# Performance work log

Measured on AMD Instinct MI355X. Metric: run time of the kernel, lower is better.

## Reference

```python
import jax, jax.numpy as jnp
import numpy as np

K = 3
STRIDE = 1
PAD = 1
DIL = 1


def setup_inputs() -> dict:
    key = jax.random.key(0)
    k1, k2, k3 = jax.random.split(key, 3)
    B, C, O, H, W = 8, 64, 64, 128, 128
    x = jax.random.normal(k1, (B, C, H, W), dtype=jnp.float32)
    # small offset-conv weights so predicted offsets stay in a sane range
    w_off = jax.random.normal(k2, (2 * K * K, C, K, K), dtype=jnp.float32) * 0.05
    b_off = jnp.zeros((2 * K * K,), dtype=jnp.float32)
    w_conv = jax.random.normal(k3, (O, C, K, K), dtype=jnp.float32) * (1.0 / np.sqrt(C * K * K))
    return {"x": x, "w_off": w_off, "b_off": b_off, "w_conv": w_conv}


def _offset_conv(x, w, b):
    y = jax.lax.conv_general_dilated(
        x, w, window_strides=(STRIDE, STRIDE),
        padding=[(PAD, PAD), (PAD, PAD)], rhs_dilation=(DIL, DIL),
        dimension_numbers=("NCHW", "OIHW", "NCHW"))
    return y + b[None, :, None, None]


def _deform_conv2d(x, offset, weight):
    # torchvision deform_conv2d v1, groups=1, offset_groups=1, no bias
    B, C, H, W = x.shape
    Ho, Wo = offset.shape[2], offset.shape[3]
    # offset channels laid out as (ky, kx, [dy, dx]) pairs
    off = offset.reshape(B, K, K, 2, Ho, Wo)
    dy, dx = off[:, :, :, 0], off[:, :, :, 1]           # [B,K,K,Ho,Wo]

    hs = (jnp.arange(Ho) * STRIDE - PAD).astype(offset.dtype)
    ws = (jnp.arange(Wo) * STRIDE - PAD).astype(offset.dtype)
    kk = (jnp.arange(K) * DIL).astype(offset.dtype)
    py = hs[None, None, None, :, None] + kk[None, :, None, None, None] + dy
    px = ws[None, None, None, None, :] + kk[None, None, :, None, None] + dx

    y0 = jnp.floor(py)
    x0 = jnp.floor(px)
    ly = py - y0
    lx = px - x0
    y0i = y0.astype(jnp.int32)
    x0i = x0.astype(jnp.int32)

    xf = x.reshape(B, C, H * W)

    def gather(yi, xi):
        valid = ((yi >= 0) & (yi < H) & (xi >= 0) & (xi < W)).astype(x.dtype)
        idx = jnp.clip(yi, 0, H - 1) * W + jnp.clip(xi, 0, W - 1)  # [B,K,K,Ho,Wo]
        idxf = idx.reshape(B, 1, -1)
        v = jnp.take_along_axis(xf, idxf, axis=2)                  # [B,C,K*K*Ho*Wo]
        v = v.reshape(B, C, K, K, Ho, Wo)
        return v * valid[:, None]                                  # zero-pad out of bounds

    ly_ = ly[:, None]  # broadcast over channel dim
    lx_ = lx[:, None]
    val = (gather(y0i, x0i) * (1 - ly_) * (1 - lx_)
           + gather(y0i, x0i + 1) * (1 - ly_) * lx_
           + gather(y0i + 1, x0i) * ly_ * (1 - lx_)
           + gather(y0i + 1, x0i + 1) * ly_ * lx_)   # [B,C,K,K,Ho,Wo]

    return jnp.einsum("bcklhw,ockl->bohw", val, weight)


def reference(x, w_off, b_off, w_conv):
    offset = _offset_conv(x, w_off, b_off)
    return _deform_conv2d(x, offset, w_conv)
```

## Files before the change

### kernel.cpp

```cpp
#include <hip/hip_runtime.h>

#define B_    8
#define C_    64
#define O_    64
#define H_    128
#define W_    128
#define HW_   (H_ * W_)
#define NOFF_ 18
#define KK_   9

typedef __attribute__((ext_vector_type(8))) _Float16 f16x8;
typedef __attribute__((ext_vector_type(2))) _Float16 f16x2;
typedef __attribute__((ext_vector_type(4))) unsigned int u32x4;
typedef __attribute__((ext_vector_type(4))) float f32x4;
typedef unsigned int uint32;
typedef unsigned short ushort;

__device__ __forceinline__ f16x2 u2h(uint32 u) {
    union { uint32 u; f16x2 h; } c; c.u = u; return c.h;
}
__device__ __forceinline__ f16x8 u2h8(u32x4 q) {
    union { u32x4 u; f16x8 h; } c; c.u = q; return c.h;
}

#define GLOAD16(dst, a64) \
    asm volatile("global_load_dwordx4 %0, %1, off" : "=&v"(dst) : "v"(a64) : "memory")
#define WAITV(N) do { \
    asm volatile("s_waitcnt vmcnt(" #N ")" ::: "memory"); \
    __builtin_amdgcn_sched_barrier(0); } while (0)
#define WAITLGKM0() do { \
    asm volatile("s_waitcnt lgkmcnt(0)" ::: "memory"); \
    __builtin_amdgcn_sched_barrier(0); } while (0)
#define DRAIN_ALL() do { \
    asm volatile("s_waitcnt vmcnt(0) lgkmcnt(0)" ::: "memory"); \
    __builtin_amdgcn_sched_barrier(0); } while (0)

__global__ __launch_bounds__(256) void transpose_x(
    const float* __restrict__ x, _Float16* __restrict__ xT)
{
    __shared__ float tile[64][65];
    int blk = blockIdx.x;
    int b   = blk >> 8;
    int hw0 = (blk & 255) * 64;
    int t   = threadIdx.x;
    int q   = t >> 6;
    int ln  = t & 63;
#pragma unroll
    for (int p = 0; p < 16; ++p) {
        int c = p * 4 + q;
        tile[c][ln] = x[((size_t)(b * C_ + c) << 14) + hw0 + ln];
    }
    __syncthreads();
#pragma unroll
    for (int p = 0; p < 16; ++p) {
        int hw = p * 4 + q;
        xT[(((size_t)b << 14) + hw0 + hw) * 64 + ln] = (_Float16)tile[ln][hw];
    }
}

__global__ __launch_bounds__(256) void prep3(
    const float* __restrict__ w_conv, const float* __restrict__ w_off,
    _Float16* __restrict__ wfrag, _Float16* __restrict__ wofff)
{
    int idx = blockIdx.x * 256 + threadIdx.x;
    if (idx < 36864) {
        int i    = idx & 7;
        int lane = (idx >> 3) & 63;
        int nb   = (idx >> 9) & 3;
        int kc   = (idx >> 11) & 1;
        int kk   = idx >> 12;
        int c = kc * 32 + ((lane >> 4) << 3) + i;
        int o = nb * 16 + (lane & 15);
        wfrag[idx] = (_Float16)w_conv[(o * C_ + c) * 9 + kk];
    }
    if (idx < 18432) {
        int i    = idx & 7;
        int lane = (idx >> 3) & 63;
        int nb   = (idx >> 9) & 1;
        int kc   = (idx >> 10) & 1;
        int kk   = idx >> 11;
        int m = nb * 16 + (lane & 15);
        int c = kc * 32 + ((lane >> 4) << 3) + i;
        wofff[idx] = (_Float16)((m < NOFF_) ? w_off[(m * C_ + c) * 9 + kk] : 0.0f);
    }
}

__global__ __launch_bounds__(512, 2) void offconv_mfma5(
    const _Float16* __restrict__ xT, const _Float16* __restrict__ wofff,
    const float* __restrict__ b_off, _Float16* __restrict__ offsh)
{
    __shared__ _Float16 wlds[18432];
    int t = threadIdx.x;
    {
        const u32x4* src = (const u32x4*)wofff;
        u32x4* dst = (u32x4*)wlds;
#pragma unroll
        for (int r = 0; r < 5; ++r) {
            int i = r * 512 + t;
            if (i < 2304) dst[i] = src[i];
        }
    }
    DRAIN_ALL();
    __syncthreads();

    int blk  = blockIdx.x;
    int b    = blk & 7;
    int hw0  = (blk >> 3) * 128;
    int lane = t & 63;
    int wv   = t >> 6;
    int pxb  = hw0 + wv * 16;
    int pr   = lane & 15;
    int g    = lane >> 4;
    int px   = pxb + pr;
    int h = px >> 7, w = px & (W_ - 1);
    const _Float16* xb = xT + (((size_t)b << 14) << 6);

    f32x4 acc[2];
#pragma unroll
    for (int nb = 0; nb < 2; ++nb) acc[nb] = (f32x4){0.f, 0.f, 0.f, 0.f};

    u32x4 q[3][2];
    bool  vld[3];

    auto issueO = [&](int kk, int st) {
        int ky = kk / 3, kx = kk % 3;
        int yy = h - 1 + ky, xx = w - 1 + kx;
        vld[st] = ((unsigned)yy < (unsigned)H_) && ((unsigned)xx < (unsigned)W_);
        int src = (min(max(yy, 0), H_ - 1) << 7) + min(max(xx, 0), W_ - 1);
        unsigned long long a = (unsigned long long)(xb + ((size_t)src << 6) + g * 8);
        GLOAD16(q[st][0], a);
        unsigned long long a2 = a + 64;
        GLOAD16(q[st][1], a2);
    };

    issueO(0, 0); issueO(1, 1); issueO(2, 2);
#pragma unroll
    for (int kk = 0; kk < KK_; ++kk) {
        const int s = kk % 3;
        if (kk < 7)      { WAITV(4); }
        else if (kk < 8) { WAITV(2); }
        else             { WAITV(0); }
#pragma unroll
        for (int kc = 0; kc < 2; ++kc) {
            f16x8 a = u2h8(q[s][kc]);
            f16x8 z = {};
            a = vld[s] ? a : z;
#pragma unroll
            for (int nb = 0; nb < 2; ++nb) {
                f16x8 bfr = *(const f16x8*)(wlds +
                    ((((kk * 2 + kc) << 1) + nb) << 9) + (lane << 3));
                acc[nb] = __builtin_amdgcn_mfma_f32_16x16x32_f16(a, bfr, acc[nb], 0, 0, 0);
            }
        }
        if (kk < 6) issueO(kk + 3, s);
    }

#pragma unroll
    for (int nb = 0; nb < 2; ++nb) {
        int m = nb * 16 + pr;
        if (m < NOFF_) {
            float bias = b_off[m];
#pragma unroll
            for (int r = 0; r < 4; ++r) {
                int prow = pxb + g * 4 + r;
                offsh[(size_t)((b << 14) + prow) * NOFF_ + m] = (_Float16)(acc[nb][r] + bias);
            }
        }
    }
}

__global__ __launch_bounds__(256, 3) void deform_mfma8(
    const _Float16* __restrict__ xT, const _Float16* __restrict__ offsh,
    const _Float16* __restrict__ wfrag, float* __restrict__ out)
{
    __shared__ _Float16 wlds[20480];
    __shared__ _Float16 val[4][1024];

    int t    = threadIdx.x;
    int blk  = blockIdx.x;
    int b    = blk & 7;
    int hw0  = (blk >> 3) * 64;
    int lane = t & 63;
    int wv   = t >> 6;
    int pxb  = hw0 + wv * 16;
    int pr   = lane & 15;
    int gg   = lane >> 4;
    int gp   = lane >> 3;
    int cg   = lane & 7;
    const _Float16* xb = xT + (((size_t)b << 14) << 6);

    {
        const u32x4* src = (const u32x4*)wfrag;
        u32x4* dst = (u32x4*)wlds;
#pragma unroll
        for (int r = 0; r < 10; ++r) dst[r * 256 + t] = src[r * 256 + t];
    }
    const uint32* obu = (const uint32*)(offsh + (size_t)((b << 14) + pxb + pr) * NOFF_);
    uint32 dpk[9];
#pragma unroll
    for (int kk = 0; kk < 9; ++kk) dpk[kk] = obu[kk];
    DRAIN_ALL();
    __syncthreads();

    f32x4 acc[4];
#pragma unroll
    for (int nb = 0; nb < 4; ++nb) acc[nb] = (f32x4){0.f, 0.f, 0.f, 0.f};

    u32x4 q[2][8];
    u32x4 wq[8];
    f16x2 Wc[2][2][4];

    auto pi = [&](int kk, int st) {
        int ky = kk / 3, kx = kk % 3;
#pragma unroll
        for (int h2 = 0; h2 < 2; ++h2) {
            int p = pxb + h2 * 8 + gp;
            uint32 du = __shfl(dpk[kk], h2 * 8 + gp, 64);
            union { uint32 u; f16x2 hh; } cv; cv.u = du;
            float dyv = (float)cv.hh[0], dxv = (float)cv.hh[1];
            int hp = p >> 7, wp = p & (W_ - 1);
            float py  = (float)(hp - 1 + ky) + dyv;
            float pxf = (float)(wp - 1 + kx) + dxv;
            float y0f = floorf(py), x0f = floorf(pxf);
            float ly = py - y0f, lx = pxf - x0f;
            int y0 = (int)y0f, x0 = (int)x0f;
            float w00 = (1.f - ly) * (1.f - lx);
            float w01 = (1.f - ly) * lx;
            float w10 = ly * (1.f - lx);
            float w11 = ly * lx;
            bool vy0 = (unsigned)y0       < (unsigned)H_;
            bool vy1 = (unsigned)(y0 + 1) < (unsigned)H_;
            bool vx0 = (unsigned)x0       < (unsigned)W_;
            bool vx1 = (unsigned)(x0 + 1) < (unsigned)W_;
            if (!(vy0 && vx0)) w00 = 0.f;
            if (!(vy0 && vx1)) w01 = 0.f;
            if (!(vy1 && vx0)) w10 = 0.f;
            if (!(vy1 && vx1)) w11 = 0.f;
            int yc0 = min(max(y0, 0), H_ - 1);
            int yc1 = min(max(y0 + 1, 0), H_ - 1);
            int xc0 = min(max(x0, 0), W_ - 1);
            int xc1 = min(max(x0 + 1, 0), W_ - 1);
            Wc[st][h2][0] = (f16x2){(_Float16)w00, (_Float16)w00};
            Wc[st][h2][1] = (f16x2){(_Float16)w01, (_Float16)w01};
            Wc[st][h2][2] = (f16x2){(_Float16)w10, (_Float16)w10};
            Wc[st][h2][3] = (f16x2){(_Float16)w11, (_Float16)w11};
            unsigned long long base = (unsigned long long)xb + ((unsigned long long)cg << 4);
            uint32 o00 = ((uint32)((yc0 << 7) + xc0)) << 7;
            uint32 o01 = ((uint32)((yc0 << 7) + xc1)) << 7;
            uint32 o10 = ((uint32)((yc1 << 7) + xc0)) << 7;
            uint32 o11 = ((uint32)((yc1 << 7) + xc1)) << 7;
            GLOAD16(q[st][h2 * 4 + 0], base + o00);
            GLOAD16(q[st][h2 * 4 + 1], base + o01);
            GLOAD16(q[st][h2 * 4 + 2], base + o10);
            GLOAD16(q[st][h2 * 4 + 3], base + o11);
        }
    };

    char* mv = (char*)val[wv];

    pi(0, 0);
#pragma unroll
    for (int kk = 0; kk < KK_; ++kk) {
        const int s = kk & 1, n = s ^ 1;

        if (kk >= 5) {
#pragma unroll
            for (int f = 0; f < 8; ++f) {
                int kc = f >> 2, nb = f & 3;
                unsigned long long wa = (unsigned long long)(wfrag +
                    ((((kk * 2 + kc) << 2) + nb) << 9) + (lane << 3));
                GLOAD16(wq[f], wa);
            }
        }
        if (kk < 8) pi(kk + 1, n);
        if (kk < 8) { WAITV(8); } else { WAITV(0); }

#pragma unroll
        for (int h2 = 0; h2 < 2; ++h2) {
            f16x8 r;
            f16x2* rp = (f16x2*)&r;
#pragma unroll
            for (int p4 = 0; p4 < 4; ++p4) {
                rp[p4] = u2h(q[s][h2 * 4 + 0][p4]) * Wc[s][h2][0]
                       + u2h(q[s][h2 * 4 + 1][p4]) * Wc[s][h2][1]
                       + u2h(q[s][h2 * 4 + 2][p4]) * Wc[s][h2][2]
                       + u2h(q[s][h2 * 4 + 3][p4]) * Wc[s][h2][3];
            }
            int pxw = h2 * 8 + gp;
            int wb  = (pxw << 7) + (cg << 4);
            *(f16x8*)(mv + (wb ^ ((pxw & 7) << 4))) = r;
        }
        WAITLGKM0();

        f16x8 a0 = *(const f16x8*)(mv + (((pr << 7) + (gg << 4))      ^ ((pr & 7) << 4)));
        f16x8 a1 = *(const f16x8*)(mv + (((pr << 7) + 64 + (gg << 4)) ^ ((pr & 7) << 4)));

#pragma unroll
        for (int kc = 0; kc < 2; ++kc) {
            f16x8 a = kc ? a1 : a0;
#pragma unroll
            for (int nb = 0; nb < 4; ++nb) {
                f16x8 bfr;
                if (kk < 5) {
                    bfr = *(const f16x8*)(wlds +
                        ((((kk * 2 + kc) << 2) + nb) << 9) + (lane << 3));
                } else {
                    bfr = u2h8(wq[kc * 4 + nb]);
                }
                acc[nb] = __builtin_amdgcn_mfma_f32_16x16x32_f16(a, bfr, acc[nb], 0, 0, 0);
            }
        }
    }

#pragma unroll
    for (int nb = 0; nb < 4; ++nb) {
        int o = nb * 16 + pr;
        float* outp = out + (((size_t)(b * O_ + o)) << 14) + pxb + (gg << 2);
        *(f32x4*)outp = acc[nb];
    }
}

extern "C" void kernel_launch(void* const* d_in, const int* in_sizes, int n_in,
                              void* d_out, int out_size, void* d_ws, size_t ws_size,
                              hipStream_t stream)
{
    const float* x      = (const float*)d_in[0];
    const float* w_off  = (const float*)d_in[1];
    const float* b_off  = (const float*)d_in[2];
    const float* w_conv = (const float*)d_in[3];
    float* out = (float*)d_out;
    char* ws = (char*)d_ws;

    const size_t XT_OFF    = 0;
    const size_t OFFS_OFF  = 16777216;
    const size_t WFRAG_OFF = 21495808;
    const size_t WOFF_OFF  = 21569536;

    _Float16* xT    = (_Float16*)(ws + XT_OFF);
    _Float16* offsh = (_Float16*)(ws + OFFS_OFF);
    _Float16* wfrag = (_Float16*)(ws + WFRAG_OFF);
    _Float16* wofff = (_Float16*)(ws + WOFF_OFF);

    transpose_x  <<<2048, 256, 0, stream>>>(x, xT);
    prep3        <<<144, 256, 0, stream>>>(w_conv, w_off, wfrag, wofff);
    offconv_mfma5<<<1024, 512, 0, stream>>>(xT, wofff, b_off, offsh);
    deform_mfma8 <<<2048, 256, 0, stream>>>(xT, offsh, wfrag, out);
}
```

Baseline: 70.76 us.

## Drop manual asm pipelining and LDS weight staging in deform kernel

Rewrites the deformable-conv kernel to use plain C++ loads in place of inline-asm global loads and manual vmcnt waits. It removes the double-buffered prefetch of the next tap and the shared-memory copy of the conv weights, reading every weight fragment from global/L2 on each tap. It also drops the occupancy hint in launch_bounds. This frees LDS and registers and hands scheduling to the compiler, at the cost of losing explicit overlap between gathers and compute and adding repeated weight reads from global memory. It also relies on compiler-inserted waits being correct now that the explicit lgkmcnt wait before the LDS reads is gone.

```diff
diff --git a/kernel.cpp b/kernel.cpp
--- a/kernel.cpp
+++ b/kernel.cpp
@@ -27,9 +27,6 @@
     asm volatile("global_load_dwordx4 %0, %1, off" : "=&v"(dst) : "v"(a64) : "memory")
 #define WAITV(N) do { \
     asm volatile("s_waitcnt vmcnt(" #N ")" ::: "memory"); \
-    __builtin_amdgcn_sched_barrier(0); } while (0)
-#define WAITLGKM0() do { \
-    asm volatile("s_waitcnt lgkmcnt(0)" ::: "memory"); \
     __builtin_amdgcn_sched_barrier(0); } while (0)
 #define DRAIN_ALL() do { \
     asm volatile("s_waitcnt vmcnt(0) lgkmcnt(0)" ::: "memory"); \
@@ -169,11 +166,10 @@
     }
 }
 
-__global__ __launch_bounds__(256, 3) void deform_mfma8(
+__global__ __launch_bounds__(256) void deform_mfma15(
     const _Float16* __restrict__ xT, const _Float16* __restrict__ offsh,
     const _Float16* __restrict__ wfrag, float* __restrict__ out)
 {
-    __shared__ _Float16 wlds[20480];
     __shared__ _Float16 val[4][1024];
 
     int t    = threadIdx.x;
@@ -189,29 +185,23 @@
     int cg   = lane & 7;
     const _Float16* xb = xT + (((size_t)b << 14) << 6);
 
-    {
-        const u32x4* src = (const u32x4*)wfrag;
-        u32x4* dst = (u32x4*)wlds;
-#pragma unroll
-        for (int r = 0; r < 10; ++r) dst[r * 256 + t] = src[r * 256 + t];
-    }
     const uint32* obu = (const uint32*)(offsh + (size_t)((b << 14) + pxb + pr) * NOFF_);
     uint32 dpk[9];
 #pragma unroll
     for (int kk = 0; kk < 9; ++kk) dpk[kk] = obu[kk];
-    DRAIN_ALL();
-    __syncthreads();
 
     f32x4 acc[4];
 #pragma unroll
     for (int nb = 0; nb < 4; ++nb) acc[nb] = (f32x4){0.f, 0.f, 0.f, 0.f};
 
-    u32x4 q[2][8];
-    u32x4 wq[8];
-    f16x2 Wc[2][2][4];
-
-    auto pi = [&](int kk, int st) {
-        int ky = kk / 3, kx = kk % 3;
+    char* mv = (char*)val[wv];
+
+#pragma unroll
+    for (int kk = 0; kk < KK_; ++kk) {
+        const int ky = kk / 3, kx = kk % 3;
+        u32x4 q[8];
+        f16x2 Wc[2][4];
+
 #pragma unroll
         for (int h2 = 0; h2 < 2; ++h2) {
             int p = pxb + h2 * 8 + gp;
@@ -240,40 +230,23 @@
             int yc1 = min(max(y0 + 1, 0), H_ - 1);
             int xc0 = min(max(x0, 0), W_ - 1);
             int xc1 = min(max(x0 + 1, 0), W_ - 1);
-            Wc[st][h2][0] = (f16x2){(_Float16)w00, (_Float16)w00};
-            Wc[st][h2][1] = (f16x2){(_Float16)w01, (_Float16)w01};
-            Wc[st][h2][2] = (f16x2){(_Float16)w10, (_Float16)w10};
-            Wc[st][h2][3] = (f16x2){(_Float16)w11, (_Float16)w11};
-            unsigned long long base = (unsigned long long)xb + ((unsigned long long)cg << 4);
-            uint32 o00 = ((uint32)((yc0 << 7) + xc0)) << 7;
-            uint32 o01 = ((uint32)((yc0 << 7) + xc1)) << 7;
-            uint32 o10 = ((uint32)((yc1 << 7) + xc0)) << 7;
-            uint32 o11 = ((uint32)((yc1 << 7) + xc1)) << 7;
-            GLOAD16(q[st][h2 * 4 + 0], base + o00);
-            GLOAD16(q[st][h2 * 4 + 1], base + o01);
-            GLOAD16(q[st][h2 * 4 + 2], base + o10);
-            GLOAD16(q[st][h2 * 4 + 3], base + o11);
-        }
-    };
-
-    char* mv = (char*)val[wv];
-
-    pi(0, 0);
-#pragma unroll
-    for (int kk = 0; kk < KK_; ++kk) {
-        const int s = kk & 1, n = s ^ 1;
-
-        if (kk >= 5) {
-#pragma unroll
-            for (int f = 0; f < 8; ++f) {
-                int kc = f >> 2, nb = f & 3;
-                unsigned long long wa = (unsigned long long)(wfrag +
-                    ((((kk * 2 + kc) << 2) + nb) << 9) + (lane << 3));
-                GLOAD16(wq[f], wa);
-            }
-        }
-        if (kk < 8) pi(kk + 1, n);
-        if (kk < 8) { WAITV(8); } else { WAITV(0); }
+            Wc[h2][0] = (f16x2){(_Float16)w00, (_Float16)w00};
+            Wc[h2][1] = (f16x2){(_Float16)w01, (_Float16)w01};
+            Wc[h2][2] = (f16x2){(_Float16)w10, (_Float16)w10};
+            Wc[h2][3] = (f16x2){(_Float16)w11, (_Float16)w11};
+            const _Float16* base = xb + cg * 8;
+            q[h2 * 4 + 0] = *(const u32x4*)(base + ((size_t)((yc0 << 7) + xc0) << 6));
+            q[h2 * 4 + 1] = *(const u32x4*)(base + ((size_t)((yc0 << 7) + xc1) << 6));
+            q[h2 * 4 + 2] = *(const u32x4*)(base + ((size_t)((yc1 << 7) + xc0) << 6));
+            q[h2 * 4 + 3] = *(const u32x4*)(base + ((size_t)((yc1 << 7) + xc1) << 6));
+        }
+
+        u32x4 wq[8];
+#pragma unroll
+        for (int f = 0; f < 8; ++f) {
+            wq[f] = *(const u32x4*)(wfrag +
+                ((((kk * 2 + (f >> 2)) << 2) + (f & 3)) << 9) + (lane << 3));
+        }
 
 #pragma unroll
         for (int h2 = 0; h2 < 2; ++h2) {
@@ -281,35 +254,25 @@
             f16x2* rp = (f16x2*)&r;
 #pragma unroll
             for (int p4 = 0; p4 < 4; ++p4) {
-                rp[p4] = u2h(q[s][h2 * 4 + 0][p4]) * Wc[s][h2][0]
-                       + u2h(q[s][h2 * 4 + 1][p4]) * Wc[s][h2][1]
-                       + u2h(q[s][h2 * 4 + 2][p4]) * Wc[s][h2][2]
-                       + u2h(q[s][h2 * 4 + 3][p4]) * Wc[s][h2][3];
+                rp[p4] = u2h(q[h2 * 4 + 0][p4]) * Wc[h2][0]
+                       + u2h(q[h2 * 4 + 1][p4]) * Wc[h2][1]
+                       + u2h(q[h2 * 4 + 2][p4]) * Wc[h2][2]
+                       + u2h(q[h2 * 4 + 3][p4]) * Wc[h2][3];
             }
             int pxw = h2 * 8 + gp;
             int wb  = (pxw << 7) + (cg << 4);
             *(f16x8*)(mv + (wb ^ ((pxw & 7) << 4))) = r;
         }
-        WAITLGKM0();
 
         f16x8 a0 = *(const f16x8*)(mv + (((pr << 7) + (gg << 4))      ^ ((pr & 7) << 4)));
         f16x8 a1 = *(const f16x8*)(mv + (((pr << 7) + 64 + (gg << 4)) ^ ((pr & 7) << 4)));
 
 #pragma unroll
-        for (int kc = 0; kc < 2; ++kc) {
-            f16x8 a = kc ? a1 : a0;
-#pragma unroll
-            for (int nb = 0; nb < 4; ++nb) {
-                f16x8 bfr;
-                if (kk < 5) {
-                    bfr = *(const f16x8*)(wlds +
-                        ((((kk * 2 + kc) << 2) + nb) << 9) + (lane << 3));
-                } else {
-                    bfr = u2h8(wq[kc * 4 + nb]);
-                }
-                acc[nb] = __builtin_amdgcn_mfma_f32_16x16x32_f16(a, bfr, acc[nb], 0, 0, 0);
-            }
-        }
+        for (int nb = 0; nb < 4; ++nb)
+            acc[nb] = __builtin_amdgcn_mfma_f32_16x16x32_f16(a0, u2h8(wq[nb]), acc[nb], 0, 0, 0);
+#pragma unroll
+        for (int nb = 0; nb < 4; ++nb)
+            acc[nb] = __builtin_amdgcn_mfma_f32_16x16x32_f16(a1, u2h8(wq[4 + nb]), acc[nb], 0, 0, 0);
     }
 
 #pragma unroll
@@ -344,5 +307,5 @@
     transpose_x  <<<2048, 256, 0, stream>>>(x, xT);
     prep3        <<<144, 256, 0, stream>>>(w_conv, w_off, wfrag, wofff);
     offconv_mfma5<<<1024, 512, 0, stream>>>(xT, wofff, b_off, offsh);
-    deform_mfma8 <<<2048, 256, 0, stream>>>(xT, offsh, wfrag, out);
-}
+    deform_mfma15<<<2048, 256, 0, stream>>>(xT, offsh, wfrag, out);
+}
```

Result: slower. 78.83 us (+11.4%).
